# Optimization experiments

Measured on AMD Instinct MI355X. Metric: run time of the kernel, lower is better.

The kernel has to match this reference:

```python
import jax, jax.numpy as jnp
import numpy as np

N, T, H = 307, 256, 64
NH, DH = 4, 16  # transformer heads, head dim (64/4)


def _layernorm(x, g, b, eps=1e-5):
    mu = x.mean(-1, keepdims=True)
    var = ((x - mu) ** 2).mean(-1, keepdims=True)
    return (x - mu) / jnp.sqrt(var + eps) * g + b


def _run_cell(x, m, tf, tj, Anorm, W0, b0, W1, mixW, mixb, Wih, Whh, bih, bhh, outW, outb, jamW, jamb):
    # x,m,tf,tj: [N,T]. Per-timestep 4-path ChebConv(K=2) + softmax mixing + GRUCell.
    hidden = Whh.shape[1]

    def step(h, xs):
        x_t, m_t, tf_t, tj_t = xs  # each [N]
        msg_in = jnp.concatenate([h, m_t[:, None], tf_t[:, None], tj_t[:, None]], axis=-1)  # [N,H+3]
        am = Anorm @ msg_in  # [N,H+3]
        m_all = jnp.tanh(jnp.einsum('ni,poi->npo', msg_in, W0) + b0
                         + jnp.einsum('ni,poi->npo', am, W1))  # [N,4,H]
        mix = jax.nn.softmax(h @ mixW.T + mixb, axis=1)  # [N,4]
        msg = jnp.einsum('np,npo->no', mix, m_all)  # [N,H]
        inp = jnp.concatenate([msg, (x_t * m_t)[:, None], m_t[:, None]], axis=-1)  # [N,H+2]
        # PyTorch GRUCell (gate order r,z,n)
        gi = inp @ Wih.T + bih
        gh = h @ Whh.T + bhh
        i_r, i_z, i_n = jnp.split(gi, 3, axis=-1)
        h_r, h_z, h_n = jnp.split(gh, 3, axis=-1)
        r = jax.nn.sigmoid(i_r + h_r)
        z = jax.nn.sigmoid(i_z + h_z)
        n = jnp.tanh(i_n + r * h_n)
        h_new = (1.0 - z) * n + z * h
        h2 = h_new + 0.1 * h
        pred = (h2 @ outW.T + outb)[:, 0]
        jam = (h2 @ jamW.T + jamb)[:, 0]
        return h2, (pred, jam, h2)

    h0 = jnp.zeros((x.shape[0], hidden), x.dtype)
    _, (preds, jams, hs) = jax.lax.scan(step, h0, (x.T, m.T, tf.T, tj.T))
    return preds.T, jams.T, jnp.transpose(hs, (1, 0, 2))  # [N,T],[N,T],[N,T,H]


def _pos_enc(Tlen, hdim, dtype):
    pos = jnp.arange(Tlen, dtype=dtype)[:, None]
    div = 10000.0 ** (jnp.arange(0, hdim, 2, dtype=dtype) / hdim)
    pe = jnp.zeros((Tlen, hdim), dtype)
    pe = pe.at[:, 0::2].set(jnp.sin(pos / div))
    pe = pe.at[:, 1::2].set(jnp.cos(pos / div))
    return pe


def _enhancer(h, qkvW, qkvb, oW, ob, g1, be1, f1W, f1b, f2W, f2b, g2, be2, pW, pb):
    # h: [N,T,H]; post-norm TransformerEncoder (relu, no dropout at eval), then Linear(H,1)
    x = h + _pos_enc(h.shape[1], h.shape[2], h.dtype)[None]
    n_layers = qkvW.shape[0]
    for l in range(n_layers):
        qkv = x @ qkvW[l].T + qkvb[l]
        q, k, v = jnp.split(qkv, 3, axis=-1)
        sh = (x.shape[0], x.shape[1], NH, DH)
        q, k, v = q.reshape(sh), k.reshape(sh), v.reshape(sh)
        att = jax.nn.softmax(jnp.einsum('nqhd,nkhd->nhqk', q, k) / np.sqrt(DH).astype(np.float32), axis=-1)
        o = jnp.einsum('nhqk,nkhd->nqhd', att, v).reshape(x.shape)
        o = o @ oW[l].T + ob[l]
        x = _layernorm(x + o, g1[l], be1[l])
        f = jax.nn.relu(x @ f1W[l].T + f1b[l]) @ f2W[l].T + f2b[l]
        x = _layernorm(x + f, g2[l], be2[l])
    return (x @ pW.T + pb)[..., 0]  # [N,T]


def _forward(x_seq, m_seq, tod_free, tod_jam, Anorm,
             cell_chebW0, cell_chebb0, cell_chebW1, cell_mixW, cell_mixb,
             cell_Wih, cell_Whh, cell_bih, cell_bhh,
             cell_outW, cell_outb, cell_jamW, cell_jamb,
             fuse_W1, fuse_b1, fuse_W2, fuse_b2,
             tr_qkvW, tr_qkvb, tr_oW, tr_ob, tr_ln1g, tr_ln1b,
             tr_ff1W, tr_ff1b, tr_ff2W, tr_ff2b, tr_ln2g, tr_ln2b,
             tr_projW, tr_projb):
    def cell(i, x, m, tf, tj):
        return _run_cell(x, m, tf, tj, Anorm,
                         cell_chebW0[i], cell_chebb0[i], cell_chebW1[i],
                         cell_mixW[i], cell_mixb[i],
                         cell_Wih[i], cell_Whh[i], cell_bih[i], cell_bhh[i],
                         cell_outW[i], cell_outb[i], cell_jamW[i], cell_jamb[i])

    flip = lambda a: a[:, ::-1]
    pf, jf, h_fwd = cell(0, x_seq, m_seq, tod_free, tod_jam)
    pb_r, jb_r, h_bwd_r = cell(1, flip(x_seq), flip(m_seq), flip(tod_free), flip(tod_jam))
    pb, jb, h_bwd = flip(pb_r), flip(jb_r), h_bwd_r[:, ::-1]

    fuse_in = jnp.stack([pf, pb], axis=-1)  # [N,T,2]
    w = jax.nn.softmax(jax.nn.relu(fuse_in @ fuse_W1.T + fuse_b1) @ fuse_W2.T + fuse_b2, axis=-1)
    speed = w[..., 0] * pf + w[..., 1] * pb
    jam_logit = w[..., 0] * jf + w[..., 1] * jb

    h_fused = h_fwd * w[..., 0:1] + h_bwd * w[..., 1:2]  # [N,T,H]
    args = lambda i: (tr_qkvW[i], tr_qkvb[i], tr_oW[i], tr_ob[i], tr_ln1g[i], tr_ln1b[i],
                      tr_ff1W[i], tr_ff1b[i], tr_ff2W[i], tr_ff2b[i], tr_ln2g[i], tr_ln2b[i],
                      tr_projW[i], tr_projb[i])
    speed_refined = _enhancer(h_fused, *args(0))
    jam_refined = _enhancer(h_fused, *args(1))
    alpha = 0.3
    speed = (1.0 - alpha) * speed + alpha * speed_refined
    jam_logit = (1.0 - alpha) * jam_logit + alpha * jam_refined
    return speed, jam_logit


def setup_inputs() -> dict:
    key = jax.random.key(0)
    keys = list(jax.random.split(key, 40))
    kit = iter(keys)

    def rn(shape, s=0.05):
        return s * jax.random.normal(next(kit), shape, jnp.float32)

    # sparse gaussian-normalized adjacency -> row-normalized diffusion matrix
    rng = np.random.default_rng(0)
    d = rng.uniform(0.5, 3.0, (N, N)); d = (d + d.T) / 2
    keep = rng.uniform(size=(N, N)) < 0.05; keep = keep | keep.T
    d = np.where(keep, d, np.inf)
    sigma = d[d < np.inf].std() + 1e-8
    adj = np.where(d < np.inf, np.exp(-d ** 2 / sigma ** 2), 0.0)
    np.fill_diagonal(adj, 1.0)
    dinv = np.where(adj.sum(1) > 0, (adj.sum(1) + 1e-8) ** -0.5, 0.0)
    adj_sym = adj * dinv[:, None] * dinv[None, :]
    rowsum = adj_sym.sum(1)
    Anorm = (adj_sym * np.where(rowsum > 0, 1.0 / rowsum, 0.0)[:, None]).astype(np.float32)

    inp = {
        'x_seq': jax.random.normal(next(kit), (N, T), jnp.float32),
        'm_seq': (jax.random.uniform(next(kit), (N, T)) < 0.5).astype(jnp.float32),
        'tod_free': jax.random.uniform(next(kit), (N, T), jnp.float32),
        'tod_jam': jax.random.uniform(next(kit), (N, T), jnp.float32),
        'Anorm': jnp.asarray(Anorm),
        'cell_chebW0': rn((2, 4, H, H + 3)), 'cell_chebb0': jnp.zeros((2, 4, H), jnp.float32),
        'cell_chebW1': rn((2, 4, H, H + 3)),
        'cell_mixW': rn((2, 4, H)), 'cell_mixb': jnp.zeros((2, 4), jnp.float32),
        'cell_Wih': rn((2, 3 * H, H + 2)), 'cell_Whh': rn((2, 3 * H, H)),
        'cell_bih': jnp.zeros((2, 3 * H), jnp.float32), 'cell_bhh': jnp.zeros((2, 3 * H), jnp.float32),
        'cell_outW': rn((2, 1, H)), 'cell_outb': jnp.zeros((2, 1), jnp.float32),
        'cell_jamW': rn((2, 1, H)), 'cell_jamb': jnp.zeros((2, 1), jnp.float32),
        'fuse_W1': rn((H, 2)), 'fuse_b1': jnp.zeros((H,), jnp.float32),
        'fuse_W2': rn((2, H)), 'fuse_b2': jnp.zeros((2,), jnp.float32),
        'tr_qkvW': rn((2, 3, 3 * H, H)), 'tr_qkvb': jnp.zeros((2, 3, 3 * H), jnp.float32),
        'tr_oW': rn((2, 3, H, H)), 'tr_ob': jnp.zeros((2, 3, H), jnp.float32),
        'tr_ln1g': jnp.ones((2, 3, H), jnp.float32), 'tr_ln1b': jnp.zeros((2, 3, H), jnp.float32),
        'tr_ff1W': rn((2, 3, 256, H)), 'tr_ff1b': jnp.zeros((2, 3, 256), jnp.float32),
        'tr_ff2W': rn((2, 3, H, 256)), 'tr_ff2b': jnp.zeros((2, 3, H), jnp.float32),
        'tr_ln2g': jnp.ones((2, 3, H), jnp.float32), 'tr_ln2b': jnp.zeros((2, 3, H), jnp.float32),
        'tr_projW': rn((2, 1, H)), 'tr_projb': jnp.zeros((2, 1), jnp.float32),
    }
    return inp


def reference(x_seq, m_seq, tod_free, tod_jam, Anorm,
              cell_chebW0, cell_chebb0, cell_chebW1, cell_mixW, cell_mixb,
              cell_Wih, cell_Whh, cell_bih, cell_bhh,
              cell_outW, cell_outb, cell_jamW, cell_jamb,
              fuse_W1, fuse_b1, fuse_W2, fuse_b2,
              tr_qkvW, tr_qkvb, tr_oW, tr_ob, tr_ln1g, tr_ln1b,
              tr_ff1W, tr_ff1b, tr_ff2W, tr_ff2b, tr_ln2g, tr_ln2b,
              tr_projW, tr_projb):
    return _forward(x_seq, m_seq, tod_free, tod_jam, Anorm,
                    cell_chebW0, cell_chebb0, cell_chebW1, cell_mixW, cell_mixb,
                    cell_Wih, cell_Whh, cell_bih, cell_bhh,
                    cell_outW, cell_outb, cell_jamW, cell_jamb,
                    fuse_W1, fuse_b1, fuse_W2, fuse_b2,
                    tr_qkvW, tr_qkvb, tr_oW, tr_ob, tr_ln1g, tr_ln1b,
                    tr_ff1W, tr_ff1b, tr_ff2W, tr_ff2b, tr_ln2g, tr_ln2b,
                    tr_projW, tr_projb)
```

## Files before the change

kernel.cpp:

```cpp
#include <hip/hip_runtime.h>
#include <math.h>

#define NN   307
#define TT   256
#define HHH  64
#define NROW (NN*TT)
#define NBLK_D 77
#define SCANB  154

typedef unsigned short u16;
typedef __attribute__((ext_vector_type(8))) short short8;
typedef __attribute__((ext_vector_type(4))) float f4;

__device__ __forceinline__ float wsum(float v){
#pragma unroll
  for (int off = 32; off > 0; off >>= 1) v += __shfl_xor(v, off, 64);
  return v;
}
__device__ __forceinline__ float wsum16(float v){
#pragma unroll
  for (int off = 8; off > 0; off >>= 1) v += __shfl_xor(v, off, 64);
  return v;
}
__device__ __forceinline__ float ftanh(float x){
  x = fminf(20.f, fmaxf(-20.f, x));
  float e = __expf(2.f*x);
  return (e - 1.f)/(e + 1.f);
}
__device__ __forceinline__ float fsigm(float x){ return 1.f/(1.f + __expf(-x)); }

__device__ __forceinline__ u16 f2bf(float x){
  unsigned u = __float_as_uint(x);
  u += 0x7fffu + ((u >> 16) & 1u);
  return (u16)(u >> 16);
}
__device__ __forceinline__ float bf2f(u16 h){
  return __uint_as_float((unsigned)h << 16);
}
__device__ __forceinline__ void split8(const float* xv, short8& hi, short8& lo){
  union { short8 v; u16 u[8]; } H, L;
#pragma unroll
  for (int j = 0; j < 8; j++){
    const float x = xv[j];
    const u16 h = f2bf(x);
    H.u[j] = h;
    L.u[j] = f2bf(x - bf2f(h));
  }
  hi = H.v; lo = L.v;
}

__global__ void k_sparse(const float* __restrict__ A, int* __restrict__ cnt,
                         int* __restrict__ idx, float* __restrict__ val){
  int n = blockIdx.x*64 + threadIdx.x;
  if (n >= NN) return;
  int c = 0;
  for (int m = 0; m < NN; m++){
    float a = A[n*NN + m];
    if (a != 0.f){ idx[n*NN + c] = m; val[n*NN + c] = a; c++; }
  }
  cnt[n] = c;
}

__global__ void k_tr_cheb(const float* __restrict__ W0, const float* __restrict__ W1,
                          float* __restrict__ W0T, float* __restrict__ W1T){
  int t = blockIdx.x*256 + threadIdx.x;
  if (t >= 2*67*256) return;
  int c = t & 255; int rest = t >> 8; int i = rest % 67; int d = rest / 67;
  int p = c >> 6, o = c & 63;
  int src = ((d*4 + p)*64 + o)*67 + i;
  W0T[t] = W0[src];
  W1T[t] = W1[src];
}

__global__ void k_tr_gru(const float* __restrict__ Wih, const float* __restrict__ Whh,
                         float* __restrict__ WihT, float* __restrict__ WhhT){
  int t = blockIdx.x*256 + threadIdx.x;
  if (t < 2*66*192){
    int j = t % 192; int rest = t / 192; int i = rest % 66; int d = rest / 66;
    WihT[t] = Wih[(d*192 + j)*66 + i];
  }
  if (t < 2*64*192){
    int j = t % 192; int rest = t / 192; int i = rest % 64; int d = rest / 64;
    WhhT[t] = Whh[(d*192 + j)*64 + i];
  }
}

__global__ void k_af(const float* __restrict__ mseq, const float* __restrict__ tfr,
                     const float* __restrict__ tjm, const int* __restrict__ cnt,
                     const int* __restrict__ idx, const float* __restrict__ val,
                     float* __restrict__ AF){
  int n = blockIdx.x, c = blockIdx.y, t = threadIdx.x;
  const float* feat = (c == 0) ? mseq : (c == 1) ? tfr : tjm;
  float acc = 0.f; int k = cnt[n];
  for (int s = 0; s < k; s++) acc += val[n*NN + s] * feat[idx[n*NN + s]*TT + t];
  AF[((size_t)c*NN + n)*TT + t] = acc;
}

__global__ void k_split(const float* __restrict__ src, u16* __restrict__ hi,
                        u16* __restrict__ lo, int n){
  int i = blockIdx.x*256 + threadIdx.x;
  if (i >= n) return;
  const float x = src[i];
  const u16 h = f2bf(x);
  hi[i] = h;
  lo[i] = f2bf(x - bf2f(h));
}

__global__ __launch_bounds__(256, 1)
void k_scan(const float* __restrict__ xseq, const float* __restrict__ mseq,
            const float* __restrict__ tfr, const float* __restrict__ tjm,
            const float* __restrict__ W0T, const float* __restrict__ W1T,
            const float* __restrict__ b0g,
            const float* __restrict__ mixW, const float* __restrict__ mixb,
            const float* __restrict__ WihT, const float* __restrict__ WhhT,
            const float* __restrict__ bih, const float* __restrict__ bhh,
            const float* __restrict__ outW, const float* __restrict__ outb,
            const float* __restrict__ jamW, const float* __restrict__ jamb,
            const int* __restrict__ spcnt, const int* __restrict__ spidx,
            const float* __restrict__ spval, const float* __restrict__ AF,
            float* __restrict__ Hseq, float* __restrict__ PRED, float* __restrict__ JPRED,
            int* __restrict__ slots)
{
  const int tid = threadIdx.x;
  const int bid = blockIdx.x;
  const int d   = bid / NBLK_D;
  const int n0  = (bid % NBLK_D) * 4;
  const int lane = tid & 63;
  const int wid  = tid >> 6;

  __shared__ __align__(16) float hsT[64][4];
  __shared__ __align__(16) float amsT[68][4];
  __shared__ __align__(16) float msgsT[64][4];
  __shared__ float malls[256][5];
  __shared__ float gis[4][192];
  __shared__ float ghs[4][192];
  __shared__ float mixs[4][4];
  __shared__ float xss[4], mss[4], tfs[4], tjs[4];
  __shared__ int   s_idx[4][320];
  __shared__ float s_val[4][320];
  __shared__ int   s_cnt[4];

  float w0r[67], w1r[67];
#pragma unroll
  for (int i = 0; i < 67; i++){
    w0r[i] = W0T[(d*67 + i)*256 + tid];
    w1r[i] = W1T[(d*67 + i)*256 + tid];
  }
  const float b0r = b0g[d*256 + tid];
  float wih_r[64], whh_r[64];
  float wih64 = 0.f, wih65 = 0.f, bih_r = 0.f, bhh_r = 0.f;
  if (tid < 192){
#pragma unroll
    for (int i = 0; i < 64; i++){
      whh_r[i] = WhhT[(d*64 + i)*192 + tid];
      wih_r[i] = WihT[(d*66 + i)*192 + tid];
    }
    wih64 = WihT[(d*66 + 64)*192 + tid];
    wih65 = WihT[(d*66 + 65)*192 + tid];
    bih_r = bih[d*192 + tid];
    bhh_r = bhh[d*192 + tid];
  }
  float mixw_r[4];
#pragma unroll
  for (int p = 0; p < 4; p++) mixw_r[p] = mixW[(d*4 + p)*64 + lane];
  const float mixb0 = mixb[d*4+0], mixb1 = mixb[d*4+1], mixb2 = mixb[d*4+2], mixb3 = mixb[d*4+3];
  const float outw_r = outW[d*64 + lane], jamw_r = jamW[d*64 + lane];
  const float outb_r = outb[d], jamb_r = jamb[d];

  for (int r = 0; r < 4; r++){
    const int n = min(n0 + r, NN-1);
    const int cc = spcnt[n];
    const int ccp = (cc + 15) & ~15;
    if (tid == 0) s_cnt[r] = ccp;
    for (int s = tid; s < ccp; s += 256){
      s_idx[r][s] = (s < cc) ? spidx[n*NN + s] : 0;
      s_val[r][s] = (s < cc) ? spval[n*NN + s] : 0.f;
    }
  }
  hsT[lane][wid] = 0.f;
  __syncthreads();

#pragma unroll 1
  for (int k = 0; k < TT; k++){
    const int ts = (d == 0) ? k : (TT-1 - k);
    if (tid < 4){
      const int r = tid; const int n = min(n0 + r, NN-1);
      const float mv = mseq[n*TT + ts];
      mss[r] = mv; tfs[r] = tfr[n*TT + ts]; tjs[r] = tjm[n*TT + ts];
      xss[r] = xseq[n*TT + ts];
      amsT[64][r] = AF[(0*NN + n)*TT + ts];
      amsT[65][r] = AF[(1*NN + n)*TT + ts];
      amsT[66][r] = AF[(2*NN + n)*TT + ts];
    }
    {
      const int r = wid;
      const float hv = hsT[lane][r];
      float l0 = wsum(hv * mixw_r[0]) + mixb0;
      float l1 = wsum(hv * mixw_r[1]) + mixb1;
      float l2 = wsum(hv * mixw_r[2]) + mixb2;
      float l3 = wsum(hv * mixw_r[3]) + mixb3;
      const float mx = fmaxf(fmaxf(l0,l1), fmaxf(l2,l3));
      const float e0 = __expf(l0-mx), e1 = __expf(l1-mx), e2 = __expf(l2-mx), e3 = __expf(l3-mx);
      const float inv = 1.f/(e0+e1+e2+e3);
      if (lane == 0){
        mixs[0][r] = e0*inv; mixs[1][r] = e1*inv; mixs[2][r] = e2*inv; mixs[3][r] = e3*inv;
      }
    }
    __syncthreads();
    {
      float a0 = b0r, a1 = b0r, a2 = b0r, a3 = b0r;
#pragma unroll
      for (int i = 0; i < 64; i++){
        const float4 h4 = *(const float4*)&hsT[i][0];
        const float w = w0r[i];
        a0 += h4.x*w; a1 += h4.y*w; a2 += h4.z*w; a3 += h4.w*w;
      }
      a0 += mss[0]*w0r[64] + tfs[0]*w0r[65] + tjs[0]*w0r[66];
      a1 += mss[1]*w0r[64] + tfs[1]*w0r[65] + tjs[1]*w0r[66];
      a2 += mss[2]*w0r[64] + tfs[2]*w0r[65] + tjs[2]*w0r[66];
      a3 += mss[3]*w0r[64] + tfs[3]*w0r[65] + tjs[3]*w0r[66];
      malls[tid][0] = a0; malls[tid][1] = a1; malls[tid][2] = a2; malls[tid][3] = a3;
    }
    if (tid < 192){
      float g0 = bhh_r, g1 = bhh_r, g2 = bhh_r, g3 = bhh_r;
#pragma unroll
      for (int i = 0; i < 64; i++){
        const float4 h4 = *(const float4*)&hsT[i][0];
        const float w = whh_r[i];
        g0 += h4.x*w; g1 += h4.y*w; g2 += h4.z*w; g3 += h4.w*w;
      }
      ghs[0][tid] = g0; ghs[1][tid] = g1; ghs[2][tid] = g2; ghs[3][tid] = g3;
      gis[0][tid] = bih_r + (xss[0]*mss[0])*wih64 + mss[0]*wih65;
      gis[1][tid] = bih_r + (xss[1]*mss[1])*wih64 + mss[1]*wih65;
      gis[2][tid] = bih_r + (xss[2]*mss[2])*wih64 + mss[2]*wih65;
      gis[3][tid] = bih_r + (xss[3]*mss[3])*wih64 + mss[3]*wih65;
    }
    if (k > 0 && tid < 64){
      const int* sl = slots + (size_t)d*NBLK_D*16;
      const int i2 = lane + 64;
      for (;;){
        const int va = (lane < NBLK_D)
            ? __hip_atomic_load(&sl[lane*16], __ATOMIC_RELAXED, __HIP_MEMORY_SCOPE_AGENT)
            : 0x7fffffff;
        const int vb = (i2 < NBLK_D)
            ? __hip_atomic_load(&sl[i2*16], __ATOMIC_RELAXED, __HIP_MEMORY_SCOPE_AGENT)
            : 0x7fffffff;
        if (__all(min(va, vb) >= k)) break;
        __builtin_amdgcn_s_sleep(1);
      }
    }
    __syncthreads();
    {
      const float* Hprev = Hseq + (size_t)(d*257 + k)*NN*64;
      const int r = wid;
      const int ccp = s_cnt[r];
      float acc = 0.f;
      for (int s = 0; s < ccp; s += 16){
        float aV[16], hV[16];
#pragma unroll
        for (int u = 0; u < 16; u++){
          const int m = s_idx[r][s+u];
          aV[u] = s_val[r][s+u];
          hV[u] = __hip_atomic_load(&Hprev[(size_t)m*64 + lane],
                                    __ATOMIC_RELAXED, __HIP_MEMORY_SCOPE_AGENT);
        }
#pragma unroll
        for (int u = 0; u < 16; u++) acc += aV[u]*hV[u];
      }
      amsT[lane][r] = acc;
    }
    __syncthreads();
    {
      const int p = tid >> 6;
      float pa0 = malls[tid][0], pa1 = malls[tid][1], pa2 = malls[tid][2], pa3 = malls[tid][3];
#pragma unroll
      for (int i = 0; i < 67; i++){
        const float4 m4 = *(const float4*)&amsT[i][0];
        const float w = w1r[i];
        pa0 += m4.x*w; pa1 += m4.y*w; pa2 += m4.z*w; pa3 += m4.w*w;
      }
      malls[tid][0] = mixs[p][0]*ftanh(pa0);
      malls[tid][1] = mixs[p][1]*ftanh(pa1);
      malls[tid][2] = mixs[p][2]*ftanh(pa2);
      malls[tid][3] = mixs[p][3]*ftanh(pa3);
    }
    __syncthreads();
    msgsT[lane][wid] = malls[lane][wid] + malls[64+lane][wid] + malls[128+lane][wid] + malls[192+lane][wid];
    __syncthreads();
    if (tid < 192){
      float q0 = gis[0][tid], q1 = gis[1][tid], q2 = gis[2][tid], q3 = gis[3][tid];
#pragma unroll
      for (int i = 0; i < 64; i++){
        const float4 m4 = *(const float4*)&msgsT[i][0];
        const float w = wih_r[i];
        q0 += m4.x*w; q1 += m4.y*w; q2 += m4.z*w; q3 += m4.w*w;
      }
      gis[0][tid] = q0; gis[1][tid] = q1; gis[2][tid] = q2; gis[3][tid] = q3;
    }
    __syncthreads();
    {
      const int r = wid, o = lane;
      const float ir = gis[r][o], iz = gis[r][o+64], in_ = gis[r][o+128];
      const float hr = ghs[r][o], hz = ghs[r][o+64], hn = ghs[r][o+128];
      const float rr2 = fsigm(ir + hr);
      const float zz = fsigm(iz + hz);
      const float nnv = ftanh(in_ + rr2*hn);
      const float hold = hsT[o][r];
      const float h2 = (1.f - zz)*nnv + zz*hold + 0.1f*hold;
      hsT[o][r] = h2;
      const int n = n0 + r;
      if (n < NN)
        __hip_atomic_store(&Hseq[((size_t)(d*257 + k + 1)*NN + n)*64 + o], h2,
                           __ATOMIC_RELAXED, __HIP_MEMORY_SCOPE_AGENT);
    }
    __syncthreads();
    if (tid == 0)
      __hip_atomic_store(&slots[bid*16], k + 1, __ATOMIC_RELAXED, __HIP_MEMORY_SCOPE_AGENT);
    {
      const float h2 = hsT[lane][wid];
      const float pv = wsum(h2 * outw_r);
      const float jv = wsum(h2 * jamw_r);
      const int n = n0 + wid;
      if (lane == 0 && n < NN){
        PRED [(d*NN + n)*TT + ts] = pv + outb_r;
        JPRED[(d*NN + n)*TT + ts] = jv + jamb_r;
      }
    }
  }
}

__global__ __launch_bounds__(256)
void k_fusion(const float* __restrict__ PRED, const float* __restrict__ JPRED,
              const float* __restrict__ Hseq,
              const float* __restrict__ fw1, const float* __restrict__ fb1,
              const float* __restrict__ fw2, const float* __restrict__ fb2,
              float* __restrict__ x0, float* __restrict__ outp)
{
  const int tid = threadIdx.x;
  const int rr = tid >> 6, lane = tid & 63;
  const int idx = blockIdx.x*4 + rr;
  const int n = idx >> 8, t = idx & 255;
  const float pf = PRED[(0*NN + n)*TT + t], pb = PRED[(NN + n)*TT + t];
  const float jf = JPRED[(0*NN + n)*TT + t], jb = JPRED[(NN + n)*TT + t];
  const float hid = fmaxf(fw1[lane*2]*pf + fw1[lane*2+1]*pb + fb1[lane], 0.f);
  const float l0 = wsum(hid * fw2[lane]) + fb2[0];
  const float l1 = wsum(hid * fw2[64+lane]) + fb2[1];
  const float mx = fmaxf(l0,l1);
  const float e0 = __expf(l0-mx), e1 = __expf(l1-mx);
  const float inv = 1.f/(e0+e1);
  const float w0 = e0*inv, w1 = e1*inv;
  const float hf = Hseq[((size_t)(0*257 + t + 1)*NN + n)*64 + lane];
  const float hb = Hseq[((size_t)(257 + 256 - t)*NN + n)*64 + lane];
  const int i2 = lane & ~1;
  const float dv = powf(10000.f, (float)i2 * (1.f/64.f));
  const float arg = (float)t / dv;
  const float pe = (lane & 1) ? cosf(arg) : sinf(arg);
  x0[(size_t)idx*64 + lane] = hf*w0 + hb*w1 + pe;
  if (lane == 0){
    outp[idx]        = 0.7f*(w0*pf + w1*pb);
    outp[NROW + idx] = 0.7f*(w0*jf + w1*jb);
  }
}

__global__ __launch_bounds__(256)
void k_qkattn(const float* __restrict__ X,
              const u16* __restrict__ Whi, const u16* __restrict__ Wlo,
              const float* __restrict__ bias, float* __restrict__ O)
{
  __shared__ __align__(16) u16 Xhi[256][72];
  __shared__ __align__(16) u16 Vt [4][16][280];
  __shared__ __align__(16) u16 Pst[4][16][264];
  __shared__ __align__(16) u16 Kscr[4][16][24];
  __shared__ __align__(16) u16 Qhs[4][16][24];
  __shared__ __align__(16) u16 Qls[4][16][24];
  const int n = blockIdx.x;
  const int tid = threadIdx.x;
  const int h = tid >> 6;
  const int l = tid & 63;
  const int m16 = l & 15, q = l >> 4;
  const float* xbase = X + (size_t)n*256*64;
  const short8 z8 = {0,0,0,0,0,0,0,0};

  {
    const float* xr = xbase + (size_t)tid*64;
#pragma unroll
    for (int c = 0; c < 64; c += 8){
      float v[8];
      *(float4*)&v[0] = *(const float4*)&xr[c];
      *(float4*)&v[4] = *(const float4*)&xr[c+4];
      union { short8 s; u16 u[8]; } pk;
#pragma unroll
      for (int j = 0; j < 8; j++) pk.u[j] = f2bf(v[j]);
      *(short8*)&Xhi[tid][c] = pk.s;
    }
  }
  __syncthreads();

  short8 WqH[2], WqL[2], WkH[2], WkL[2], WvH[2], WvL[2];
#pragma unroll
  for (int kh = 0; kh < 2; kh++){
    const size_t rq = (size_t)(h*16 + m16)*64 + kh*32 + q*8;
    const size_t rk = (size_t)(64 + h*16 + m16)*64 + kh*32 + q*8;
    const size_t rv = (size_t)(128 + h*16 + m16)*64 + kh*32 + q*8;
    WqH[kh] = *(const short8*)&Whi[rq]; WqL[kh] = *(const short8*)&Wlo[rq];
    WkH[kh] = *(const short8*)&Whi[rk]; WkL[kh] = *(const short8*)&Wlo[rk];
    WvH[kh] = *(const short8*)&Whi[rv]; WvL[kh] = *(const short8*)&Wlo[rv];
  }
  const float qb = bias[h*16 + m16];
  const float kb = bias[64 + h*16 + m16];
  const float vb = bias[128 + h*16 + m16];

  short8 Kb[16];
#pragma unroll 1
  for (int ct = 0; ct < 16; ct++){
    short8 Xa0 = *(const short8*)&Xhi[ct*16 + m16][q*8];
    short8 Xa1 = *(const short8*)&Xhi[ct*16 + m16][32 + q*8];
    f4 ka = {0.f,0.f,0.f,0.f}, va = {0.f,0.f,0.f,0.f};
    ka = __builtin_amdgcn_mfma_f32_16x16x32_bf16(Xa0, WkH[0], ka, 0, 0, 0);
    ka = __builtin_amdgcn_mfma_f32_16x16x32_bf16(Xa0, WkL[0], ka, 0, 0, 0);
    ka = __builtin_amdgcn_mfma_f32_16x16x32_bf16(Xa1, WkH[1], ka, 0, 0, 0);
    ka = __builtin_amdgcn_mfma_f32_16x16x32_bf16(Xa1, WkL[1], ka, 0, 0, 0);
    va = __builtin_amdgcn_mfma_f32_16x16x32_bf16(Xa0, WvH[0], va, 0, 0, 0);
    va = __builtin_amdgcn_mfma_f32_16x16x32_bf16(Xa0, WvL[0], va, 0, 0, 0);
    va = __builtin_amdgcn_mfma_f32_16x16x32_bf16(Xa1, WvH[1], va, 0, 0, 0);
    va = __builtin_amdgcn_mfma_f32_16x16x32_bf16(Xa1, WvL[1], va, 0, 0, 0);
#pragma unroll
    for (int r = 0; r < 4; r++){
      Kscr[h][q*4 + r][m16] = f2bf(ka[r] + kb);
      Vt[h][m16][ct*16 + q*4 + r] = f2bf(va[r] + vb);
    }
    Kb[ct] = (q < 2) ? *(const short8*)&Kscr[h][m16][q*8] : z8;
  }

#pragma unroll 1
  for (int c = 0; c < 16; c++){
    short8 Xa0 = *(const short8*)&Xhi[c*16 + m16][q*8];
    short8 Xa1 = *(const short8*)&Xhi[c*16 + m16][32 + q*8];
    f4 qa = {0.f,0.f,0.f,0.f};
    qa = __builtin_amdgcn_mfma_f32_16x16x32_bf16(Xa0, WqH[0], qa, 0, 0, 0);
    qa = __builtin_amdgcn_mfma_f32_16x16x32_bf16(Xa0, WqL[0], qa, 0, 0, 0);
    qa = __builtin_amdgcn_mfma_f32_16x16x32_bf16(Xa1, WqH[1], qa, 0, 0, 0);
    qa = __builtin_amdgcn_mfma_f32_16x16x32_bf16(Xa1, WqL[1], qa, 0, 0, 0);
#pragma unroll
    for (int r = 0; r < 4; r++){
      const float qv = (qa[r] + qb) * 0.25f;
      const u16 hh = f2bf(qv);
      Qhs[h][q*4 + r][m16] = hh;
      Qls[h][q*4 + r][m16] = f2bf(qv - bf2f(hh));
    }
    short8 Qh = z8, Ql = z8;
    if (q < 2){
      Qh = *(const short8*)&Qhs[h][m16][q*8];
      Ql = *(const short8*)&Qls[h][m16][q*8];
    }
    float rs[4] = {0.f, 0.f, 0.f, 0.f};
#pragma unroll
    for (int ct = 0; ct < 16; ct++){
      f4 s = {0.f,0.f,0.f,0.f};
      s = __builtin_amdgcn_mfma_f32_16x16x32_bf16(Qh, Kb[ct], s, 0, 0, 0);
      s = __builtin_amdgcn_mfma_f32_16x16x32_bf16(Ql, Kb[ct], s, 0, 0, 0);
#pragma unroll
      for (int r = 0; r < 4; r++){
        const float p = __expf(s[r]);
        rs[r] += p;
        Pst[h][q*4 + r][ct*16 + m16] = f2bf(p);
      }
    }
#pragma unroll
    for (int r = 0; r < 4; r++) rs[r] = wsum16(rs[r]);
    f4 acc = {0.f,0.f,0.f,0.f};
#pragma unroll
    for (int kt = 0; kt < 8; kt++){
      const short8 Pa = *(const short8*)&Pst[h][m16][kt*32 + q*8];
      const short8 Vb = *(const short8*)&Vt[h][m16][kt*32 + q*8];
      acc = __builtin_amdgcn_mfma_f32_16x16x32_bf16(Pa, Vb, acc, 0, 0, 0);
    }
#pragma unroll
    for (int r = 0; r < 4; r++){
      O[((size_t)n*256 + c*16 + q*4 + r)*64 + h*16 + m16] = acc[r] / rs[r];
    }
  }
}

__global__ __launch_bounds__(256)
void k_oproj_ln(const float* __restrict__ X, const u16* __restrict__ Whi,
                const u16* __restrict__ Wlo, const float* __restrict__ bias,
                const float* __restrict__ Xres, const float* __restrict__ g,
                const float* __restrict__ b, float* __restrict__ Y)
{
  const int tid = threadIdx.x;
  const int w = tid >> 6, l = tid & 63;
  const int m16 = l & 15, q = l >> 4;
  const int row = blockIdx.x*64 + w*16 + m16;
  short8 Ah[2], Al[2];
#pragma unroll
  for (int kh = 0; kh < 2; kh++){
    float xv[8];
    *(float4*)&xv[0] = *(const float4*)&X[(size_t)row*64 + kh*32 + q*8];
    *(float4*)&xv[4] = *(const float4*)&X[(size_t)row*64 + kh*32 + q*8 + 4];
    split8(xv, Ah[kh], Al[kh]);
  }
  f4 acc[4];
#pragma unroll
  for (int nt = 0; nt < 4; nt++){
    acc[nt] = (f4){0.f, 0.f, 0.f, 0.f};
    const int n = nt*16 + m16;
#pragma unroll
    for (int kh = 0; kh < 2; kh++){
      const short8 Bh = *(const short8*)&Whi[(size_t)n*64 + kh*32 + q*8];
      const short8 Bl = *(const short8*)&Wlo[(size_t)n*64 + kh*32 + q*8];
      acc[nt] = __builtin_amdgcn_mfma_f32_16x16x32_bf16(Ah[kh], Bh, acc[nt], 0, 0, 0);
      acc[nt] = __builtin_amdgcn_mfma_f32_16x16x32_bf16(Ah[kh], Bl, acc[nt], 0, 0, 0);
      acc[nt] = __builtin_amdgcn_mfma_f32_16x16x32_bf16(Al[kh], Bh, acc[nt], 0, 0, 0);
    }
  }
  const int rbase = blockIdx.x*64 + w*16 + q*4;
#pragma unroll
  for (int r = 0; r < 4; r++){
    float v[4]; float s = 0.f;
#pragma unroll
    for (int nt = 0; nt < 4; nt++){
      const int col = nt*16 + m16;
      v[nt] = acc[nt][r] + bias[col] + Xres[(size_t)(rbase + r)*64 + col];
      s += v[nt];
    }
    const float mu = wsum16(s) * (1.f/64.f);
    float vs = 0.f;
#pragma unroll
    for (int nt = 0; nt < 4; nt++){ v[nt] -= mu; vs += v[nt]*v[nt]; }
    const float rstd = rsqrtf(wsum16(vs) * (1.f/64.f) + 1e-5f);
#pragma unroll
    for (int nt = 0; nt < 4; nt++){
      const int col = nt*16 + m16;
      Y[(size_t)(rbase + r)*64 + col] = v[nt] * rstd * g[col] + b[col];
    }
  }
}

__global__ __launch_bounds__(256)
void k_ffblock(const float* __restrict__ X,
               const u16* __restrict__ W1hi, const u16* __restrict__ W1lo,
               const float* __restrict__ b1,
               const u16* __restrict__ W2hi, const u16* __restrict__ W2lo,
               const float* __restrict__ b2,
               const float* __restrict__ g, const float* __restrict__ b,
               float* __restrict__ Y)
{
  __shared__ __align__(16) u16 Hs[64][280];
  const int tid = threadIdx.x;
  const int w = tid >> 6, l = tid & 63;
  const int m16 = l & 15, q = l >> 4;
  const int row = blockIdx.x*64 + w*16 + m16;
  short8 Ah[2], Al[2];
#pragma unroll
  for (int kh = 0; kh < 2; kh++){
    float xv[8];
    *(float4*)&xv[0] = *(const float4*)&X[(size_t)row*64 + kh*32 + q*8];
    *(float4*)&xv[4] = *(const float4*)&X[(size_t)row*64 + kh*32 + q*8 + 4];
    split8(xv, Ah[kh], Al[kh]);
  }
  for (int nt = 0; nt < 16; nt++){
    const int n = nt*16 + m16;
    f4 acc = {0.f, 0.f, 0.f, 0.f};
#pragma unroll
    for (int kh = 0; kh < 2; kh++){
      const short8 Bh = *(const short8*)&W1hi[(size_t)n*64 + kh*32 + q*8];
      const short8 Bl = *(const short8*)&W1lo[(size_t)n*64 + kh*32 + q*8];
      acc = __builtin_amdgcn_mfma_f32_16x16x32_bf16(Ah[kh], Bh, acc, 0, 0, 0);
      acc = __builtin_amdgcn_mfma_f32_16x16x32_bf16(Ah[kh], Bl, acc, 0, 0, 0);
      acc = __builtin_amdgcn_mfma_f32_16x16x32_bf16(Al[kh], Bh, acc, 0, 0, 0);
    }
    const float bb = b1[n];
#pragma unroll
    for (int r = 0; r < 4; r++){
      const float h = fmaxf(acc[r] + bb, 0.f);
      Hs[w*16 + q*4 + r][n] = f2bf(h);
    }
  }
  __syncthreads();
  f4 acc2[4];
#pragma unroll
  for (int nt = 0; nt < 4; nt++) acc2[nt] = (f4){0.f, 0.f, 0.f, 0.f};
#pragma unroll 1
  for (int kh = 0; kh < 8; kh++){
    const short8 Ahh = *(const short8*)&Hs[w*16 + m16][kh*32 + q*8];
#pragma unroll
    for (int nt = 0; nt < 4; nt++){
      const int n = nt*16 + m16;
      const short8 Bh = *(const short8*)&W2hi[(size_t)n*256 + kh*32 + q*8];
      const short8 Bl = *(const short8*)&W2lo[(size_t)n*256 + kh*32 + q*8];
      acc2[nt] = __builtin_amdgcn_mfma_f32_16x16x32_bf16(Ahh, Bh, acc2[nt], 0, 0, 0);
      acc2[nt] = __builtin_amdgcn_mfma_f32_16x16x32_bf16(Ahh, Bl, acc2[nt], 0, 0, 0);
    }
  }
  const int rbase = blockIdx.x*64 + w*16 + q*4;
#pragma unroll
  for (int r = 0; r < 4; r++){
    float v[4]; float s = 0.f;
#pragma unroll
    for (int nt = 0; nt < 4; nt++){
      const int col = nt*16 + m16;
      v[nt] = acc2[nt][r] + b2[col] + X[(size_t)(rbase + r)*64 + col];
      s += v[nt];
    }
    const float mu = wsum16(s) * (1.f/64.f);
    float vs = 0.f;
#pragma unroll
    for (int nt = 0; nt < 4; nt++){ v[nt] -= mu; vs += v[nt]*v[nt]; }
    const float rstd = rsqrtf(wsum16(vs) * (1.f/64.f) + 1e-5f);
#pragma unroll
    for (int nt = 0; nt < 4; nt++){
      const int col = nt*16 + m16;
      Y[(size_t)(rbase + r)*64 + col] = v[nt] * rstd * g[col] + b[col];
    }
  }
}

__global__ __launch_bounds__(256)
void k_proj_add(const float* __restrict__ X, const float* __restrict__ pW,
                const float* __restrict__ pb, float* __restrict__ outp)
{
  const int tid = threadIdx.x;
  const int r = tid >> 6, lane = tid & 63;
  const size_t row = (size_t)blockIdx.x*4 + r;
  const float v = X[row*64 + lane] * pW[lane];
  const float s = wsum(v);
  if (lane == 0) outp[row] += 0.3f*(s + pb[0]);
}

extern "C" void kernel_launch(void* const* d_in, const int* in_sizes, int n_in,
                              void* d_out, int out_size, void* d_ws, size_t ws_size,
                              hipStream_t stream)
{
  const float* x_seq = (const float*)d_in[0];
  const float* m_seq = (const float*)d_in[1];
  const float* tod_f = (const float*)d_in[2];
  const float* tod_j = (const float*)d_in[3];
  const float* Anorm = (const float*)d_in[4];
  const float* chW0  = (const float*)d_in[5];
  const float* chb0  = (const float*)d_in[6];
  const float* chW1  = (const float*)d_in[7];
  const float* mixW  = (const float*)d_in[8];
  const float* mixb  = (const float*)d_in[9];
  const float* Wih   = (const float*)d_in[10];
  const float* Whh   = (const float*)d_in[11];
  const float* bih   = (const float*)d_in[12];
  const float* bhh   = (const float*)d_in[13];
  const float* outW  = (const float*)d_in[14];
  const float* outbp = (const float*)d_in[15];
  const float* jamW  = (const float*)d_in[16];
  const float* jambp = (const float*)d_in[17];
  const float* fW1   = (const float*)d_in[18];
  const float* fb1   = (const float*)d_in[19];
  const float* fW2   = (const float*)d_in[20];
  const float* fb2   = (const float*)d_in[21];
  const float* qkvW  = (const float*)d_in[22];
  const float* qkvb  = (const float*)d_in[23];
  const float* oW    = (const float*)d_in[24];
  const float* ob    = (const float*)d_in[25];
  const float* ln1g  = (const float*)d_in[26];
  const float* ln1b  = (const float*)d_in[27];
  const float* f1W   = (const float*)d_in[28];
  const float* f1b   = (const float*)d_in[29];
  const float* f2W   = (const float*)d_in[30];
  const float* f2b   = (const float*)d_in[31];
  const float* ln2g  = (const float*)d_in[32];
  const float* ln2b  = (const float*)d_in[33];
  const float* prW   = (const float*)d_in[34];
  const float* prb   = (const float*)d_in[35];
  float* out = (float*)d_out;

  float* ws = (float*)d_ws;
  size_t off = 0;
  auto take = [&](size_t n)->float*{ float* p = ws + off; off += (n + 63) & ~(size_t)63; return p; };
  int*   slots = (int*)take(4096);
  float* W0T  = take((size_t)2*67*256);
  float* W1T  = take((size_t)2*67*256);
  float* WihT = take((size_t)2*66*192);
  float* WhhT = take((size_t)2*64*192);
  int*   spcnt = (int*)take(320);
  int*   spidx = (int*)take((size_t)NN*NN);
  float* spval = take((size_t)NN*NN);
  float* AF    = take((size_t)3*NN*TT);
  float* PRED  = take((size_t)2*NN*TT);
  float* JPRED = take((size_t)2*NN*TT);
  float* HSEQ  = take((size_t)2*257*NN*64);
  float* X0    = take((size_t)NROW*64);
  float* XBUF  = take((size_t)NROW*64);
  float* OBUF  = take((size_t)NROW*64);
  const size_t NQKV = (size_t)6*192*64;
  const size_t NO   = (size_t)6*64*64;
  const size_t NF1  = (size_t)6*256*64;
  const size_t NF2  = (size_t)6*64*256;
  const size_t NWTOT = NQKV + NO + NF1 + NF2;
  u16* WHI = (u16*)take((NWTOT + 1)/2);
  u16* WLO = (u16*)take((NWTOT + 1)/2);
  (void)ws_size; (void)in_sizes; (void)n_in; (void)out_size;

  hipMemsetAsync(slots, 0, 4096*sizeof(int), stream);
  hipMemsetAsync(HSEQ, 0, (size_t)NN*64*sizeof(float), stream);
  hipMemsetAsync(HSEQ + (size_t)257*NN*64, 0, (size_t)NN*64*sizeof(float), stream);

  k_sparse<<<dim3((NN+63)/64), dim3(64), 0, stream>>>(Anorm, spcnt, spidx, spval);
  k_tr_cheb<<<dim3(134), dim3(256), 0, stream>>>(chW0, chW1, W0T, W1T);
  k_tr_gru<<<dim3(99), dim3(256), 0, stream>>>(Wih, Whh, WihT, WhhT);
  k_af<<<dim3(NN,3), dim3(256), 0, stream>>>(m_seq, tod_f, tod_j, spcnt, spidx, spval, AF);
  k_split<<<dim3((int)((NQKV+255)/256)), dim3(256), 0, stream>>>(qkvW, WHI, WLO, (int)NQKV);
  k_split<<<dim3((int)((NO+255)/256)), dim3(256), 0, stream>>>(oW, WHI+NQKV, WLO+NQKV, (int)NO);
  k_split<<<dim3((int)((NF1+255)/256)), dim3(256), 0, stream>>>(f1W, WHI+NQKV+NO, WLO+NQKV+NO, (int)NF1);
  k_split<<<dim3((int)((NF2+255)/256)), dim3(256), 0, stream>>>(f2W, WHI+NQKV+NO+NF1, WLO+NQKV+NO+NF1, (int)NF2);

  k_scan<<<dim3(SCANB), dim3(256), 0, stream>>>(x_seq, m_seq, tod_f, tod_j, W0T, W1T,
      chb0, mixW, mixb, WihT, WhhT, bih, bhh, outW, outbp, jamW, jambp,
      spcnt, spidx, spval, AF, HSEQ, PRED, JPRED, slots);

  k_fusion<<<dim3(NROW/4), dim3(256), 0, stream>>>(PRED, JPRED, HSEQ, fW1, fb1, fW2, fb2, X0, out);

  for (int e = 0; e < 2; e++){
    for (int l = 0; l < 3; l++){
      const int el = e*3 + l;
      const float* xin = (l == 0) ? X0 : XBUF;
      const u16* qhi = WHI + (size_t)el*192*64;
      const u16* qlo = WLO + (size_t)el*192*64;
      const u16* ohi = WHI + NQKV + (size_t)el*64*64;
      const u16* olo = WLO + NQKV + (size_t)el*64*64;
      const u16* f1hi = WHI + NQKV + NO + (size_t)el*256*64;
      const u16* f1lo = WLO + NQKV + NO + (size_t)el*256*64;
      const u16* f2hi = WHI + NQKV + NO + NF1 + (size_t)el*64*256;
      const u16* f2lo = WLO + NQKV + NO + NF1 + (size_t)el*64*256;
      k_qkattn<<<dim3(NN), dim3(256), 0, stream>>>(xin, qhi, qlo,
          qkvb + (size_t)el*192, OBUF);
      k_oproj_ln<<<dim3(NROW/64), dim3(256), 0, stream>>>(OBUF, ohi, olo,
          ob + (size_t)el*64, xin, ln1g + (size_t)el*64, ln1b + (size_t)el*64, XBUF);
      k_ffblock<<<dim3(NROW/64), dim3(256), 0, stream>>>(XBUF, f1hi, f1lo,
          f1b + (size_t)el*256, f2hi, f2lo, f2b + (size_t)el*64,
          ln2g + (size_t)el*64, ln2b + (size_t)el*64, XBUF);
    }
    k_proj_add<<<dim3(NROW/4), dim3(256), 0, stream>>>(XBUF, prW + (size_t)e*64, prb + e,
        out + (size_t)e*NROW);
  }
}
```

Measured before the change: 4.645 ms.

## Batch both enhancer stacks per launch and move pred/jam heads out of scan

The per-step output and jam projections are removed from the sequential scan kernel and recomputed in the fusion kernel from the stored hidden states. This shortens the critical recurrent loop. The two independent transformer enhancers are also batched into single launches over a second grid dimension, with separate XBUF/OBUF buffers per enhancer. That halves the number of launches and doubles per-launch parallelism, at the cost of double workspace.

```diff
diff --git a/kernel.cpp b/kernel.cpp
--- a/kernel.cpp
+++ b/kernel.cpp
@@ -7,6 +7,11 @@
 #define NROW (NN*TT)
 #define NBLK_D 77
 #define SCANB  154
+
+#define OFF_O  (6*192*64)
+#define OFF_F1 (OFF_O + 6*64*64)
+#define OFF_F2 (OFF_F1 + 6*256*64)
+#define NWTOT  (OFF_F2 + 6*64*256)
 
 typedef unsigned short u16;
 typedef __attribute__((ext_vector_type(8))) short short8;
@@ -114,12 +119,9 @@
             const float* __restrict__ mixW, const float* __restrict__ mixb,
             const float* __restrict__ WihT, const float* __restrict__ WhhT,
             const float* __restrict__ bih, const float* __restrict__ bhh,
-            const float* __restrict__ outW, const float* __restrict__ outb,
-            const float* __restrict__ jamW, const float* __restrict__ jamb,
             const int* __restrict__ spcnt, const int* __restrict__ spidx,
             const float* __restrict__ spval, const float* __restrict__ AF,
-            float* __restrict__ Hseq, float* __restrict__ PRED, float* __restrict__ JPRED,
-            int* __restrict__ slots)
+            float* __restrict__ Hseq, int* __restrict__ slots)
 {
   const int tid = threadIdx.x;
   const int bid = blockIdx.x;
@@ -164,8 +166,6 @@
 #pragma unroll
   for (int p = 0; p < 4; p++) mixw_r[p] = mixW[(d*4 + p)*64 + lane];
   const float mixb0 = mixb[d*4+0], mixb1 = mixb[d*4+1], mixb2 = mixb[d*4+2], mixb3 = mixb[d*4+3];
-  const float outw_r = outW[d*64 + lane], jamw_r = jamW[d*64 + lane];
-  const float outb_r = outb[d], jamb_r = jamb[d];
 
   for (int r = 0; r < 4; r++){
     const int n = min(n0 + r, NN-1);
@@ -316,22 +316,13 @@
     __syncthreads();
     if (tid == 0)
       __hip_atomic_store(&slots[bid*16], k + 1, __ATOMIC_RELAXED, __HIP_MEMORY_SCOPE_AGENT);
-    {
-      const float h2 = hsT[lane][wid];
-      const float pv = wsum(h2 * outw_r);
-      const float jv = wsum(h2 * jamw_r);
-      const int n = n0 + wid;
-      if (lane == 0 && n < NN){
-        PRED [(d*NN + n)*TT + ts] = pv + outb_r;
-        JPRED[(d*NN + n)*TT + ts] = jv + jamb_r;
-      }
-    }
   }
 }
 
 __global__ __launch_bounds__(256)
-void k_fusion(const float* __restrict__ PRED, const float* __restrict__ JPRED,
-              const float* __restrict__ Hseq,
+void k_fusion(const float* __restrict__ Hseq,
+              const float* __restrict__ outW, const float* __restrict__ outb,
+              const float* __restrict__ jamW, const float* __restrict__ jamb,
               const float* __restrict__ fw1, const float* __restrict__ fb1,
               const float* __restrict__ fw2, const float* __restrict__ fb2,
               float* __restrict__ x0, float* __restrict__ outp)
@@ -340,8 +331,12 @@
   const int rr = tid >> 6, lane = tid & 63;
   const int idx = blockIdx.x*4 + rr;
   const int n = idx >> 8, t = idx & 255;
-  const float pf = PRED[(0*NN + n)*TT + t], pb = PRED[(NN + n)*TT + t];
-  const float jf = JPRED[(0*NN + n)*TT + t], jb = JPRED[(NN + n)*TT + t];
+  const float hf = Hseq[((size_t)(0*257 + t + 1)*NN + n)*64 + lane];
+  const float hb = Hseq[((size_t)(257 + 256 - t)*NN + n)*64 + lane];
+  const float pf = wsum(hf * outW[lane])      + outb[0];
+  const float pb = wsum(hb * outW[64 + lane]) + outb[1];
+  const float jf = wsum(hf * jamW[lane])      + jamb[0];
+  const float jb = wsum(hb * jamW[64 + lane]) + jamb[1];
   const float hid = fmaxf(fw1[lane*2]*pf + fw1[lane*2+1]*pb + fb1[lane], 0.f);
   const float l0 = wsum(hid * fw2[lane]) + fb2[0];
   const float l1 = wsum(hid * fw2[64+lane]) + fb2[1];
@@ -349,8 +344,6 @@
   const float e0 = __expf(l0-mx), e1 = __expf(l1-mx);
   const float inv = 1.f/(e0+e1);
   const float w0 = e0*inv, w1 = e1*inv;
-  const float hf = Hseq[((size_t)(0*257 + t + 1)*NN + n)*64 + lane];
-  const float hb = Hseq[((size_t)(257 + 256 - t)*NN + n)*64 + lane];
   const int i2 = lane & ~1;
   const float dv = powf(10000.f, (float)i2 * (1.f/64.f));
   const float arg = (float)t / dv;
@@ -363,9 +356,9 @@
 }
 
 __global__ __launch_bounds__(256)
-void k_qkattn(const float* __restrict__ X,
-              const u16* __restrict__ Whi, const u16* __restrict__ Wlo,
-              const float* __restrict__ bias, float* __restrict__ O)
+void k_qkattn(const float* __restrict__ X0, const float* __restrict__ XBUF, int lyr,
+              const u16* __restrict__ WHI, const u16* __restrict__ WLO,
+              const float* __restrict__ qkvb_all, float* __restrict__ OBUF)
 {
   __shared__ __align__(16) u16 Xhi[256][72];
   __shared__ __align__(16) u16 Vt [4][16][280];
@@ -374,6 +367,13 @@
   __shared__ __align__(16) u16 Qhs[4][16][24];
   __shared__ __align__(16) u16 Qls[4][16][24];
   const int n = blockIdx.x;
+  const int e = blockIdx.y;
+  const int el = e*3 + lyr;
+  const float* X = (lyr == 0) ? X0 : (XBUF + (size_t)e*NROW*64);
+  const u16* Whi = WHI + (size_t)el*192*64;
+  const u16* Wlo = WLO + (size_t)el*192*64;
+  const float* bias = qkvb_all + (size_t)el*192;
+  float* O = OBUF + (size_t)e*NROW*64;
   const int tid = threadIdx.x;
   const int h = tid >> 6;
   const int l = tid & 63;
@@ -483,11 +483,22 @@
 }
 
 __global__ __launch_bounds__(256)
-void k_oproj_ln(const float* __restrict__ X, const u16* __restrict__ Whi,
-                const u16* __restrict__ Wlo, const float* __restrict__ bias,
-                const float* __restrict__ Xres, const float* __restrict__ g,
-                const float* __restrict__ b, float* __restrict__ Y)
+void k_oproj_ln(const float* __restrict__ OBUF, const float* __restrict__ X0,
+                float* __restrict__ XBUF, int lyr,
+                const u16* __restrict__ WHI, const u16* __restrict__ WLO,
+                const float* __restrict__ ob_all,
+                const float* __restrict__ g_all, const float* __restrict__ b_all)
 {
+  const int e = blockIdx.y;
+  const int el = e*3 + lyr;
+  const float* X = OBUF + (size_t)e*NROW*64;
+  const float* Xres = (lyr == 0) ? X0 : (XBUF + (size_t)e*NROW*64);
+  float* Y = XBUF + (size_t)e*NROW*64;
+  const u16* Whi = WHI + OFF_O + (size_t)el*64*64;
+  const u16* Wlo = WLO + OFF_O + (size_t)el*64*64;
+  const float* bias = ob_all + (size_t)el*64;
+  const float* g = g_all + (size_t)el*64;
+  const float* b = b_all + (size_t)el*64;
   const int tid = threadIdx.x;
   const int w = tid >> 6, l = tid & 63;
   const int m16 = l & 15, q = l >> 4;
@@ -538,15 +549,23 @@
 }
 
 __global__ __launch_bounds__(256)
-void k_ffblock(const float* __restrict__ X,
-               const u16* __restrict__ W1hi, const u16* __restrict__ W1lo,
-               const float* __restrict__ b1,
-               const u16* __restrict__ W2hi, const u16* __restrict__ W2lo,
-               const float* __restrict__ b2,
-               const float* __restrict__ g, const float* __restrict__ b,
-               float* __restrict__ Y)
+void k_ffblock(float* __restrict__ XBUF, int lyr,
+               const u16* __restrict__ WHI, const u16* __restrict__ WLO,
+               const float* __restrict__ b1_all, const float* __restrict__ b2_all,
+               const float* __restrict__ g_all, const float* __restrict__ b_all)
 {
   __shared__ __align__(16) u16 Hs[64][280];
+  const int e = blockIdx.y;
+  const int el = e*3 + lyr;
+  float* X = XBUF + (size_t)e*NROW*64;
+  const u16* W1hi = WHI + OFF_F1 + (size_t)el*256*64;
+  const u16* W1lo = WLO + OFF_F1 + (size_t)el*256*64;
+  const u16* W2hi = WHI + OFF_F2 + (size_t)el*64*256;
+  const u16* W2lo = WLO + OFF_F2 + (size_t)el*64*256;
+  const float* b1 = b1_all + (size_t)el*256;
+  const float* b2 = b2_all + (size_t)el*64;
+  const float* g = g_all + (size_t)el*64;
+  const float* b = b_all + (size_t)el*64;
   const int tid = threadIdx.x;
   const int w = tid >> 6, l = tid & 63;
   const int m16 = l & 15, q = l >> 4;
@@ -611,21 +630,25 @@
 #pragma unroll
     for (int nt = 0; nt < 4; nt++){
       const int col = nt*16 + m16;
-      Y[(size_t)(rbase + r)*64 + col] = v[nt] * rstd * g[col] + b[col];
+      X[(size_t)(rbase + r)*64 + col] = v[nt] * rstd * g[col] + b[col];
     }
   }
 }
 
 __global__ __launch_bounds__(256)
-void k_proj_add(const float* __restrict__ X, const float* __restrict__ pW,
-                const float* __restrict__ pb, float* __restrict__ outp)
+void k_proj_add(const float* __restrict__ XBUF, const float* __restrict__ prW,
+                const float* __restrict__ prb, float* __restrict__ out)
 {
+  const int e = blockIdx.y;
+  const float* X = XBUF + (size_t)e*NROW*64;
+  const float* pW = prW + (size_t)e*64;
+  float* outp = out + (size_t)e*NROW;
   const int tid = threadIdx.x;
   const int r = tid >> 6, lane = tid & 63;
   const size_t row = (size_t)blockIdx.x*4 + r;
   const float v = X[row*64 + lane] * pW[lane];
   const float s = wsum(v);
-  if (lane == 0) outp[row] += 0.3f*(s + pb[0]);
+  if (lane == 0) outp[row] += 0.3f*(s + prb[e]);
 }
 
 extern "C" void kernel_launch(void* const* d_in, const int* in_sizes, int n_in,
@@ -682,20 +705,18 @@
   int*   spidx = (int*)take((size_t)NN*NN);
   float* spval = take((size_t)NN*NN);
   float* AF    = take((size_t)3*NN*TT);
-  float* PRED  = take((size_t)2*NN*TT);
-  float* JPRED = take((size_t)2*NN*TT);
   float* HSEQ  = take((size_t)2*257*NN*64);
   float* X0    = take((size_t)NROW*64);
-  float* XBUF  = take((size_t)NROW*64);
-  float* OBUF  = take((size_t)NROW*64);
+  float* XBUF  = take((size_t)2*NROW*64);
+  float* OBUF  = take((size_t)2*NROW*64);
+  u16* WHI = (u16*)take(((size_t)NWTOT + 1)/2);
+  u16* WLO = (u16*)take(((size_t)NWTOT + 1)/2);
+  (void)ws_size; (void)in_sizes; (void)n_in; (void)out_size;
+
   const size_t NQKV = (size_t)6*192*64;
   const size_t NO   = (size_t)6*64*64;
   const size_t NF1  = (size_t)6*256*64;
   const size_t NF2  = (size_t)6*64*256;
-  const size_t NWTOT = NQKV + NO + NF1 + NF2;
-  u16* WHI = (u16*)take((NWTOT + 1)/2);
-  u16* WLO = (u16*)take((NWTOT + 1)/2);
-  (void)ws_size; (void)in_sizes; (void)n_in; (void)out_size;
 
   hipMemsetAsync(slots, 0, 4096*sizeof(int), stream);
   hipMemsetAsync(HSEQ, 0, (size_t)NN*64*sizeof(float), stream);
@@ -706,37 +727,23 @@
   k_tr_gru<<<dim3(99), dim3(256), 0, stream>>>(Wih, Whh, WihT, WhhT);
   k_af<<<dim3(NN,3), dim3(256), 0, stream>>>(m_seq, tod_f, tod_j, spcnt, spidx, spval, AF);
   k_split<<<dim3((int)((NQKV+255)/256)), dim3(256), 0, stream>>>(qkvW, WHI, WLO, (int)NQKV);
-  k_split<<<dim3((int)((NO+255)/256)), dim3(256), 0, stream>>>(oW, WHI+NQKV, WLO+NQKV, (int)NO);
-  k_split<<<dim3((int)((NF1+255)/256)), dim3(256), 0, stream>>>(f1W, WHI+NQKV+NO, WLO+NQKV+NO, (int)NF1);
-  k_split<<<dim3((int)((NF2+255)/256)), dim3(256), 0, stream>>>(f2W, WHI+NQKV+NO+NF1, WLO+NQKV+NO+NF1, (int)NF2);
+  k_split<<<dim3((int)((NO+255)/256)), dim3(256), 0, stream>>>(oW, WHI+OFF_O, WLO+OFF_O, (int)NO);
+  k_split<<<dim3((int)((NF1+255)/256)), dim3(256), 0, stream>>>(f1W, WHI+OFF_F1, WLO+OFF_F1, (int)NF1);
+  k_split<<<dim3((int)((NF2+255)/256)), dim3(256), 0, stream>>>(f2W, WHI+OFF_F2, WLO+OFF_F2, (int)NF2);
 
   k_scan<<<dim3(SCANB), dim3(256), 0, stream>>>(x_seq, m_seq, tod_f, tod_j, W0T, W1T,
-      chb0, mixW, mixb, WihT, WhhT, bih, bhh, outW, outbp, jamW, jambp,
-      spcnt, spidx, spval, AF, HSEQ, PRED, JPRED, slots);
-
-  k_fusion<<<dim3(NROW/4), dim3(256), 0, stream>>>(PRED, JPRED, HSEQ, fW1, fb1, fW2, fb2, X0, out);
-
-  for (int e = 0; e < 2; e++){
-    for (int l = 0; l < 3; l++){
-      const int el = e*3 + l;
-      const float* xin = (l == 0) ? X0 : XBUF;
-      const u16* qhi = WHI + (size_t)el*192*64;
-      const u16* qlo = WLO + (size_t)el*192*64;
-      const u16* ohi = WHI + NQKV + (size_t)el*64*64;
-      const u16* olo = WLO + NQKV + (size_t)el*64*64;
-      const u16* f1hi = WHI + NQKV + NO + (size_t)el*256*64;
-      const u16* f1lo = WLO + NQKV + NO + (size_t)el*256*64;
-      const u16* f2hi = WHI + NQKV + NO + NF1 + (size_t)el*64*256;
-      const u16* f2lo = WLO + NQKV + NO + NF1 + (size_t)el*64*256;
-      k_qkattn<<<dim3(NN), dim3(256), 0, stream>>>(xin, qhi, qlo,
-          qkvb + (size_t)el*192, OBUF);
-      k_oproj_ln<<<dim3(NROW/64), dim3(256), 0, stream>>>(OBUF, ohi, olo,
-          ob + (size_t)el*64, xin, ln1g + (size_t)el*64, ln1b + (size_t)el*64, XBUF);
-      k_ffblock<<<dim3(NROW/64), dim3(256), 0, stream>>>(XBUF, f1hi, f1lo,
-          f1b + (size_t)el*256, f2hi, f2lo, f2b + (size_t)el*64,
-          ln2g + (size_t)el*64, ln2b + (size_t)el*64, XBUF);
-    }
-    k_proj_add<<<dim3(NROW/4), dim3(256), 0, stream>>>(XBUF, prW + (size_t)e*64, prb + e,
-        out + (size_t)e*NROW);
-  }
-}
+      chb0, mixW, mixb, WihT, WhhT, bih, bhh,
+      spcnt, spidx, spval, AF, HSEQ, slots);
+
+  k_fusion<<<dim3(NROW/4), dim3(256), 0, stream>>>(HSEQ, outW, outbp, jamW, jambp,
+      fW1, fb1, fW2, fb2, X0, out);
+
+  for (int l = 0; l < 3; l++){
+    k_qkattn<<<dim3(NN, 2), dim3(256), 0, stream>>>(X0, XBUF, l, WHI, WLO, qkvb, OBUF);
+    k_oproj_ln<<<dim3(NROW/64, 2), dim3(256), 0, stream>>>(OBUF, X0, XBUF, l,
+        WHI, WLO, ob, ln1g, ln1b);
+    k_ffblock<<<dim3(NROW/64, 2), dim3(256), 0, stream>>>(XBUF, l, WHI, WLO,
+        f1b, f2b, ln2g, ln2b);
+  }
+  k_proj_add<<<dim3(NROW/4, 2), dim3(256), 0, stream>>>(XBUF, prW, prb, out);
+}
```

Measured after the change: 4.351 ms. -6.3%, faster.
